# Kernel optimization log

Hardware: AMD Instinct MI355X
Metric: run time of the kernel (lower is better)

The kernel has to match this reference:

```python
import jax, jax.numpy as jnp
import numpy as np

EMBED_DIM = 1024
NUM_HEADS = 16
HEAD_DIM = EMBED_DIM // NUM_HEADS
NUM_GLOBAL = 2
NUM_RANDOM = 3
WINDOW_SIZE = 3
B, S = 2, 2048


def setup_inputs() -> dict:
    key = jax.random.key(0)
    ks = jax.random.split(key, 10)
    scale = 0.02
    inp = {
        "x": jax.random.normal(ks[0], (B, S, EMBED_DIM), dtype=jnp.float32),
        "random_indices": jax.random.randint(ks[1], (S, NUM_RANDOM), 0, S, dtype=jnp.int32),
        "q_w": jax.random.normal(ks[2], (EMBED_DIM, EMBED_DIM), dtype=jnp.float32) * scale,
        "q_b": jnp.zeros((EMBED_DIM,), dtype=jnp.float32),
        "k_w": jax.random.normal(ks[3], (EMBED_DIM, EMBED_DIM), dtype=jnp.float32) * scale,
        "k_b": jnp.zeros((EMBED_DIM,), dtype=jnp.float32),
        "v_w": jax.random.normal(ks[4], (EMBED_DIM, EMBED_DIM), dtype=jnp.float32) * scale,
        "v_b": jnp.zeros((EMBED_DIM,), dtype=jnp.float32),
        "o_w": jax.random.normal(ks[5], (EMBED_DIM, EMBED_DIM), dtype=jnp.float32) * scale,
        "o_b": jnp.zeros((EMBED_DIM,), dtype=jnp.float32),
    }
    return inp


def _build_mask(random_indices, seq_len):
    # [S, S] boolean BigBird mask: global rows/cols + sliding window + random.
    i = jnp.arange(seq_len)[:, None]
    j = jnp.arange(seq_len)[None, :]
    glob = (i < NUM_GLOBAL) | (j < NUM_GLOBAL)
    win = jnp.abs(i - j) <= WINDOW_SIZE
    rand = jnp.zeros((seq_len, seq_len), dtype=bool)
    rows = jnp.repeat(jnp.arange(seq_len), NUM_RANDOM)
    rand = rand.at[rows, random_indices.reshape(-1)].set(True)
    return glob | win | rand


def reference(x, random_indices, q_w, q_b, k_w, k_b, v_w, v_b, o_w, o_b):
    b, s, _ = x.shape
    # torch nn.Linear: y = x @ W.T + b
    q = (x @ q_w.T + q_b).reshape(b, s, NUM_HEADS, HEAD_DIM).transpose(0, 2, 1, 3)
    k = (x @ k_w.T + k_b).reshape(b, s, NUM_HEADS, HEAD_DIM).transpose(0, 2, 1, 3)
    v = (x @ v_w.T + v_b).reshape(b, s, NUM_HEADS, HEAD_DIM).transpose(0, 2, 1, 3)
    scores = jnp.einsum("bhqd,bhkd->bhqk", q, k) / jnp.sqrt(jnp.float32(HEAD_DIM))
    mask = _build_mask(random_indices, s)  # [S, S]
    scores = jnp.where(mask[None, None, :, :], scores, -jnp.inf)
    probs = jax.nn.softmax(scores, axis=-1)
    out = jnp.einsum("bhqk,bhkd->bhqd", probs, v)
    out = out.transpose(0, 2, 1, 3).reshape(b, s, EMBED_DIM)
    return out @ o_w.T + o_b
```

## Files before the change

kernel.cpp:

```cpp
#include <hip/hip_runtime.h>

#define B_  2
#define S_  2048
#define E_  1024
#define H_  16
#define D_  64
#define NGLOB 2
#define NRAND 3
#define WIN 3

typedef __bf16 bf16x8 __attribute__((ext_vector_type(8)));
typedef float  f32x4  __attribute__((ext_vector_type(4)));

__device__ __forceinline__ unsigned short f2bf(float f) {
    unsigned u = __builtin_bit_cast(unsigned, f);
    unsigned r = u + 0x7FFFu + ((u >> 16) & 1u);
    return (unsigned short)(r >> 16);
}
__device__ __forceinline__ float bf2f(unsigned short u) {
    return __builtin_bit_cast(float, (unsigned)u << 16);
}

__device__ __forceinline__ void g2l16(const unsigned short* g, unsigned short* l) {
    __builtin_amdgcn_global_load_lds(
        (const __attribute__((address_space(1))) unsigned*)g,
        (__attribute__((address_space(3))) unsigned*)l, 16, 0, 0);
}

__global__ __launch_bounds__(256)
void convert_all(const float* __restrict__ x,  const float* __restrict__ qw,
                 const float* __restrict__ kw, const float* __restrict__ vw,
                 const float* __restrict__ ow,
                 unsigned short* __restrict__ xb, unsigned short* __restrict__ wqkv,
                 unsigned short* __restrict__ wo) {
    const int XN = (B_ * S_ * E_) / 4;
    const int WN = (E_ * E_) / 4;
    int i = blockIdx.x * blockDim.x + threadIdx.x;
    int r, loc;
    if (i < XN) { r = 0; loc = i; }
    else        { int j = i - XN; r = 1 + (j >> 18); loc = j & (WN - 1); }
    const float* src = r == 0 ? x : r == 1 ? qw : r == 2 ? kw : r == 3 ? vw : ow;
    float4 f = ((const float4*)src)[loc];
    ushort4 u;
    u.x = f2bf(f.x); u.y = f2bf(f.y); u.z = f2bf(f.z); u.w = f2bf(f.w);
    ushort4* dst = r == 0 ? (ushort4*)xb : r == 4 ? (ushort4*)wo
                 : (ushort4*)wqkv + (size_t)(r - 1) * WN;
    dst[loc] = u;
}

__global__ __launch_bounds__(256, 3)
void gemm_qkv(const unsigned short* __restrict__ A,
              const unsigned short* __restrict__ W,
              const float* __restrict__ b0, const float* __restrict__ b1,
              const float* __restrict__ b2,
              unsigned short* __restrict__ Cb, int M, int N, int K) {
    __shared__ unsigned short sA[128 * 64];
    __shared__ unsigned short sB[128 * 64];
    const int t = threadIdx.x;
    const int lane = t & 63;
    const int wave = t >> 6;
    const int wm = wave >> 1, wn = wave & 1;
    const int lq = lane >> 4;
    const int lr = lane & 15;
    const int bm = blockIdx.x * 128;
    const int bn = blockIdx.y * 128;

    f32x4 acc[4][4] = {};

    for (int k0 = 0; k0 < K; k0 += 64) {
        const unsigned short* Abase = A + (size_t)bm * K + k0;
        const unsigned short* Wbase = W + (size_t)bn * K + k0;
        #pragma unroll
        for (int j = 0; j < 4; ++j) {
            int c = j * 256 + t;
            int row = c >> 3, cc = c & 7;
            int gcol = ((cc ^ (row & 7)) << 3);
            int dst = j * 2048 + wave * 512;
            g2l16(Abase + (size_t)row * K + gcol, sA + dst);
            g2l16(Wbase + (size_t)row * K + gcol, sB + dst);
        }
        __syncthreads();

        #pragma unroll
        for (int ks = 0; ks < 2; ++ks) {
            const int sw = (((ks << 2) + lq) ^ (lr & 7)) << 3;
            bf16x8 af[4], bfr[4];
            #pragma unroll
            for (int i = 0; i < 4; ++i)
                af[i] = *(const bf16x8*)&sA[(wm * 64 + i * 16 + lr) * 64 + sw];
            #pragma unroll
            for (int j = 0; j < 4; ++j)
                bfr[j] = *(const bf16x8*)&sB[(wn * 64 + j * 16 + lr) * 64 + sw];
            #pragma unroll
            for (int i = 0; i < 4; ++i)
                #pragma unroll
                for (int j = 0; j < 4; ++j)
                    acc[i][j] = __builtin_amdgcn_mfma_f32_16x16x32_bf16(af[i], bfr[j], acc[i][j], 0, 0, 0);
        }
        __syncthreads();
    }

    #pragma unroll
    for (int i = 0; i < 4; ++i) {
        int row0 = bm + wm * 64 + i * 16 + lq * 4;
        #pragma unroll
        for (int j = 0; j < 4; ++j) {
            int col = bn + wn * 64 + j * 16 + lr;
            const float* bp = col < E_ ? b0 : (col < 2 * E_ ? b1 : b2);
            float bv = bp[col & (E_ - 1)];
            #pragma unroll
            for (int r = 0; r < 4; ++r)
                Cb[(size_t)(row0 + r) * N + col] = f2bf(acc[i][j][r] + bv);
        }
    }
}

__global__ __launch_bounds__(256, 2)
void gemm_o64(const unsigned short* __restrict__ A,
              const unsigned short* __restrict__ W,
              const float* __restrict__ bias,
              float* __restrict__ Cf, int M, int N, int K) {
    __shared__ unsigned short sA[128 * 64];
    __shared__ unsigned short sB[64 * 64];
    const int t = threadIdx.x;
    const int lane = t & 63;
    const int wave = t >> 6;
    const int lq = lane >> 4;
    const int lr = lane & 15;
    const int bm = blockIdx.x * 128;
    const int bn = blockIdx.y * 64;

    f32x4 acc[2][4] = {};

    for (int k0 = 0; k0 < K; k0 += 64) {
        const unsigned short* Abase = A + (size_t)bm * K + k0;
        const unsigned short* Wbase = W + (size_t)bn * K + k0;
        #pragma unroll
        for (int j = 0; j < 4; ++j) {
            int c = j * 256 + t;
            int row = c >> 3, cc = c & 7;
            int gcol = ((cc ^ (row & 7)) << 3);
            int dst = j * 2048 + wave * 512;
            g2l16(Abase + (size_t)row * K + gcol, sA + dst);
        }
        #pragma unroll
        for (int j = 0; j < 2; ++j) {
            int c = j * 256 + t;
            int row = c >> 3, cc = c & 7;
            int gcol = ((cc ^ (row & 7)) << 3);
            int dst = j * 2048 + wave * 512;
            g2l16(Wbase + (size_t)row * K + gcol, sB + dst);
        }
        __syncthreads();

        #pragma unroll
        for (int ks = 0; ks < 2; ++ks) {
            const int sw = (((ks << 2) + lq) ^ (lr & 7)) << 3;
            bf16x8 af[2], bfr[4];
            #pragma unroll
            for (int i = 0; i < 2; ++i)
                af[i] = *(const bf16x8*)&sA[(wave * 32 + i * 16 + lr) * 64 + sw];
            #pragma unroll
            for (int j = 0; j < 4; ++j)
                bfr[j] = *(const bf16x8*)&sB[(j * 16 + lr) * 64 + sw];
            #pragma unroll
            for (int i = 0; i < 2; ++i)
                #pragma unroll
                for (int j = 0; j < 4; ++j)
                    acc[i][j] = __builtin_amdgcn_mfma_f32_16x16x32_bf16(af[i], bfr[j], acc[i][j], 0, 0, 0);
        }
        __syncthreads();
    }

    #pragma unroll
    for (int i = 0; i < 2; ++i) {
        int row0 = bm + wave * 32 + i * 16 + lq * 4;
        #pragma unroll
        for (int j = 0; j < 4; ++j) {
            int col = bn + j * 16 + lr;
            float bv = bias[col];
            #pragma unroll
            for (int r = 0; r < 4; ++r)
                Cf[(size_t)(row0 + r) * N + col] = acc[i][j][r] + bv;
        }
    }
}

__global__ __launch_bounds__(256)
void attn_fused(const unsigned short* __restrict__ qkv,
                const int* __restrict__ rnd,
                float* __restrict__ gsc, float* __restrict__ gacc,
                unsigned short* __restrict__ attn) {
    const int NB = B_ * (S_ - 2);
    int t = threadIdx.x;

    if (blockIdx.x >= 1024) {
        int bid2 = blockIdx.x - 1024;
        int tup = bid2 >> 3, seg = bid2 & 7;
        int b = tup >> 5, i = (tup >> 4) & 1, h = tup & 15;
        __shared__ float qs[D_];
        if (t < D_) qs[t] = bf2f(qkv[(size_t)(b * S_ + i) * 3072 + h * D_ + t]);
        if (seg == 0 && t < D_) gacc[tup * D_ + t] = 0.f;
        __syncthreads();
        int c = seg * 256 + t;
        const bf16x8* kp = (const bf16x8*)(qkv + (size_t)(b * S_ + c) * 3072 + E_ + h * D_);
        float s = 0.f;
        #pragma unroll
        for (int w = 0; w < 8; ++w) {
            bf16x8 kv = kp[w];
            #pragma unroll
            for (int j = 0; j < 8; ++j) s += qs[w * 8 + j] * (float)kv[j];
        }
        gsc[(size_t)tup * S_ + c] = s * 0.125f;
        return;
    }

    int bidx = (blockIdx.x & 7) * 128 + (blockIdx.x >> 3);
    int w = t >> 6, l = t & 63;
    int row = bidx * 4 + w;
    bool valid = row < NB;
    int b = row / (S_ - 2);
    int i = row % (S_ - 2) + 2;
    if (!valid) { b = 0; i = 2; }

    __shared__ int   cols_s[4][12];
    __shared__ int   ncol_sh[4];
    __shared__ float pr_s[4][16 * 13 + 3];

    const bf16x8* qp = (const bf16x8*)(qkv + (size_t)(b * S_ + i) * 3072);
    bf16x8 q0 = qp[l * 2], q1 = qp[l * 2 + 1];
    float qreg[16];
    #pragma unroll
    for (int j = 0; j < 8; ++j) { qreg[j] = (float)q0[j]; qreg[8 + j] = (float)q1[j]; }

    if (l == 0) {
        int* cols = cols_s[w];
        int n = 0;
        cols[n++] = 0; cols[n++] = 1;
        int lo = i - WIN; if (lo < NGLOB) lo = NGLOB;
        int hi = i + WIN; if (hi > S_ - 1) hi = S_ - 1;
        for (int j = lo; j <= hi; ++j) cols[n++] = j;
        for (int r = 0; r < NRAND; ++r) {
            int c = rnd[i * NRAND + r];
            bool dup = false;
            for (int q = 0; q < n; ++q) dup = dup || (cols[q] == c);
            if (!dup) cols[n++] = c;
        }
        ncol_sh[w] = n;
        for (int q = n; q < 12; ++q) cols[q] = 0;
    }
    __syncthreads();
    const int n = ncol_sh[w];
    const int h4 = l >> 2;

    float sco[12];
    #pragma unroll
    for (int c = 0; c < 12; ++c) {
        const bf16x8* kp = (const bf16x8*)(qkv + (size_t)(b * S_ + cols_s[w][c]) * 3072 + E_);
        bf16x8 k0 = kp[l * 2], k1 = kp[l * 2 + 1];
        float s = 0.f;
        #pragma unroll
        for (int j = 0; j < 8; ++j) s += qreg[j] * (float)k0[j] + qreg[8 + j] * (float)k1[j];
        s += __shfl_xor(s, 1);
        s += __shfl_xor(s, 2);
        sco[c] = (c < n) ? s * 0.125f : -1e30f;
    }

    if ((l & 3) == 0) {
        float m = -1e30f;
        #pragma unroll
        for (int c = 0; c < 12; ++c) m = fmaxf(m, sco[c]);
        float sum = 0.f;
        #pragma unroll
        for (int c = 0; c < 12; ++c) { float e = __expf(sco[c] - m); sco[c] = e; sum += e; }
        float inv = 1.f / sum;
        #pragma unroll
        for (int c = 0; c < 12; ++c) pr_s[w][h4 * 13 + c] = sco[c] * inv;
    }
    __syncthreads();

    float o[16] = {};
    #pragma unroll
    for (int c = 0; c < 12; ++c) {
        float p = pr_s[w][h4 * 13 + c];
        const bf16x8* vp = (const bf16x8*)(qkv + (size_t)(b * S_ + cols_s[w][c]) * 3072 + 2 * E_);
        bf16x8 v0 = vp[l * 2], v1 = vp[l * 2 + 1];
        #pragma unroll
        for (int j = 0; j < 8; ++j) { o[j] += p * (float)v0[j]; o[8 + j] += p * (float)v1[j]; }
    }

    if (valid) {
        ushort4 u0, u1, u2, u3;
        u0.x = f2bf(o[0]);  u0.y = f2bf(o[1]);  u0.z = f2bf(o[2]);  u0.w = f2bf(o[3]);
        u1.x = f2bf(o[4]);  u1.y = f2bf(o[5]);  u1.z = f2bf(o[6]);  u1.w = f2bf(o[7]);
        u2.x = f2bf(o[8]);  u2.y = f2bf(o[9]);  u2.z = f2bf(o[10]); u2.w = f2bf(o[11]);
        u3.x = f2bf(o[12]); u3.y = f2bf(o[13]); u3.z = f2bf(o[14]); u3.w = f2bf(o[15]);
        ushort4* op = (ushort4*)(attn + (size_t)(b * S_ + i) * E_ + l * 16);
        op[0] = u0; op[1] = u1; op[2] = u2; op[3] = u3;
    }
}

__global__ __launch_bounds__(256)
void gattn_pv(const unsigned short* __restrict__ qkv, const float* __restrict__ gsc,
              float* __restrict__ gacc) {
    int tup = blockIdx.x, chunk = blockIdx.y;
    int b = tup >> 5, h = tup & 15;
    int t = threadIdx.x, w = t >> 6, d = t & 63;
    __shared__ float ps[S_];
    __shared__ float red[4];
    __shared__ float redv[4][D_];
    const float* sc = gsc + (size_t)tup * S_;

    float vals[8];
    float m = -1e30f;
    #pragma unroll
    for (int k = 0; k < 8; ++k) { vals[k] = sc[t + 256 * k]; m = fmaxf(m, vals[k]); }
    #pragma unroll
    for (int o = 32; o; o >>= 1) m = fmaxf(m, __shfl_down(m, o));
    if ((t & 63) == 0) red[t >> 6] = m;
    __syncthreads();
    m = fmaxf(fmaxf(red[0], red[1]), fmaxf(red[2], red[3]));
    __syncthreads();
    float sum = 0.f;
    #pragma unroll
    for (int k = 0; k < 8; ++k) { float e = __expf(vals[k] - m); vals[k] = e; sum += e; }
    #pragma unroll
    for (int o = 32; o; o >>= 1) sum += __shfl_down(sum, o);
    if ((t & 63) == 0) red[t >> 6] = sum;
    __syncthreads();
    float inv = 1.f / (red[0] + red[1] + red[2] + red[3]);
    #pragma unroll
    for (int k = 0; k < 8; ++k) ps[t + 256 * k] = vals[k] * inv;
    __syncthreads();

    const float* P = ps + chunk * 256 + w * 64;
    float acc = 0.f;
    #pragma unroll 4
    for (int k = 0; k < 64; ++k) {
        int c = chunk * 256 + w * 64 + k;
        acc += P[k] * bf2f(qkv[(size_t)(b * S_ + c) * 3072 + 2 * E_ + h * D_ + d]);
    }
    redv[w][d] = acc;
    __syncthreads();
    if (w == 0)
        atomicAdd(&gacc[tup * D_ + d], redv[0][d] + redv[1][d] + redv[2][d] + redv[3][d]);
}

__global__ __launch_bounds__(256)
void gattn_fin(const float* __restrict__ gacc, unsigned short* __restrict__ attn) {
    int gid = blockIdx.x * 256 + threadIdx.x;
    int tup = gid >> 6, d = gid & 63;
    int b = tup >> 5, i = (tup >> 4) & 1, h = tup & 15;
    attn[(size_t)(b * S_ + i) * E_ + h * D_ + d] = f2bf(gacc[gid]);
}

extern "C" void kernel_launch(void* const* d_in, const int* in_sizes, int n_in,
                              void* d_out, int out_size, void* d_ws, size_t ws_size,
                              hipStream_t stream) {
    const float* x   = (const float*)d_in[0];
    const int*   rnd = (const int*)d_in[1];
    const float* qw  = (const float*)d_in[2];
    const float* qb  = (const float*)d_in[3];
    const float* kw  = (const float*)d_in[4];
    const float* kb  = (const float*)d_in[5];
    const float* vw  = (const float*)d_in[6];
    const float* vb  = (const float*)d_in[7];
    const float* ow  = (const float*)d_in[8];
    const float* ob  = (const float*)d_in[9];
    float* out = (float*)d_out;

    char* ws = (char*)d_ws;
    unsigned short* xb    = (unsigned short*)(ws);
    unsigned short* wqkv  = (unsigned short*)(ws + 8388608);
    unsigned short* wo    = (unsigned short*)(ws + 14680064);
    unsigned short* qkv   = (unsigned short*)(ws + 16777216);
    unsigned short* attn  = (unsigned short*)(ws + 41943040);
    float*          gsc   = (float*)(ws);
    float*          gacc  = (float*)(ws + 524288);

    const int M = B_ * S_;

    {
        int total4 = (M * E_ + 4 * E_ * E_) / 4;
        convert_all<<<total4 / 256, 256, 0, stream>>>(x, qw, kw, vw, ow, xb, wqkv, wo);
    }

    {
        dim3 grid(M / 128, 3 * E_ / 128);
        gemm_qkv<<<grid, 256, 0, stream>>>(xb, wqkv, qb, kb, vb, qkv, M, 3 * E_, E_);
    }

    attn_fused<<<1024 + 512, 256, 0, stream>>>(qkv, rnd, gsc, gacc, attn);

    gattn_pv<<<dim3(B_ * NGLOB * H_, S_ / 256), 256, 0, stream>>>(qkv, gsc, gacc);
    gattn_fin<<<(B_ * NGLOB * H_ * D_) / 256, 256, 0, stream>>>(gacc, attn);

    {
        dim3 grid(M / 128, E_ / 64);
        gemm_o64<<<grid, 256, 0, stream>>>(attn, wo, ob, out, M, E_, E_);
    }
}
```

Measured before the change: 173.1 us.

## Restructure QKV GEMM into 256x256 tile double-buffered pipelined kernel

```diff
diff --git a/kernel.cpp b/kernel.cpp
--- a/kernel.cpp
+++ b/kernel.cpp
@@ -48,69 +48,158 @@
     dst[loc] = u;
 }
 
-__global__ __launch_bounds__(256, 3)
+__device__ __forceinline__ void stage_half(const unsigned short* g, unsigned short* l,
+                                           int t, int wave, int K) {
+    #pragma unroll
+    for (int j = 0; j < 2; ++j) {
+        int c = j * 512 + t;
+        int row = c >> 3, cc = c & 7;
+        g2l16(g + (size_t)row * K + ((cc ^ (row & 7)) << 3), l + j * 4096 + wave * 512);
+    }
+}
+__device__ __forceinline__ bf16x8 ldfrag(const unsigned short* r, int row, int kc) {
+    return *(const bf16x8*)&r[row * 64 + ((kc ^ (row & 7)) << 3)];
+}
+
+__global__ __launch_bounds__(512, 2)
 void gemm_qkv(const unsigned short* __restrict__ A,
               const unsigned short* __restrict__ W,
-              const float* __restrict__ b0, const float* __restrict__ b1,
-              const float* __restrict__ b2,
+              const float* __restrict__ bi0, const float* __restrict__ bi1,
+              const float* __restrict__ bi2,
               unsigned short* __restrict__ Cb, int M, int N, int K) {
-    __shared__ unsigned short sA[128 * 64];
-    __shared__ unsigned short sB[128 * 64];
+    __shared__ unsigned short lds[2][4][128 * 64];
     const int t = threadIdx.x;
     const int lane = t & 63;
     const int wave = t >> 6;
-    const int wm = wave >> 1, wn = wave & 1;
+    const int wr = wave >> 2;
+    const int wc = wave & 3;
     const int lq = lane >> 4;
     const int lr = lane & 15;
-    const int bm = blockIdx.x * 128;
-    const int bn = blockIdx.y * 128;
-
-    f32x4 acc[4][4] = {};
-
-    for (int k0 = 0; k0 < K; k0 += 64) {
-        const unsigned short* Abase = A + (size_t)bm * K + k0;
-        const unsigned short* Wbase = W + (size_t)bn * K + k0;
-        #pragma unroll
-        for (int j = 0; j < 4; ++j) {
-            int c = j * 256 + t;
-            int row = c >> 3, cc = c & 7;
-            int gcol = ((cc ^ (row & 7)) << 3);
-            int dst = j * 2048 + wave * 512;
-            g2l16(Abase + (size_t)row * K + gcol, sA + dst);
-            g2l16(Wbase + (size_t)row * K + gcol, sB + dst);
-        }
-        __syncthreads();
-
-        #pragma unroll
-        for (int ks = 0; ks < 2; ++ks) {
-            const int sw = (((ks << 2) + lq) ^ (lr & 7)) << 3;
-            bf16x8 af[4], bfr[4];
-            #pragma unroll
-            for (int i = 0; i < 4; ++i)
-                af[i] = *(const bf16x8*)&sA[(wm * 64 + i * 16 + lr) * 64 + sw];
-            #pragma unroll
-            for (int j = 0; j < 4; ++j)
-                bfr[j] = *(const bf16x8*)&sB[(wn * 64 + j * 16 + lr) * 64 + sw];
-            #pragma unroll
-            for (int i = 0; i < 4; ++i)
+    const int bm = blockIdx.x * 256;
+    const int bn = blockIdx.y * 256;
+    const int nt = K >> 6;
+
+    const unsigned short* Ab = A + (size_t)bm * K;
+    const unsigned short* Wb = W + (size_t)bn * K;
+
+    f32x4 acc[8][4] = {};
+
+    stage_half(Ab,                         &lds[0][0][0], t, wave, K);
+    stage_half(Ab + (size_t)128 * K,       &lds[0][1][0], t, wave, K);
+    stage_half(Wb,                         &lds[0][2][0], t, wave, K);
+    stage_half(Wb + (size_t)128 * K,       &lds[0][3][0], t, wave, K);
+    stage_half(Wb + 64,                    &lds[1][2][0], t, wave, K);
+    stage_half(Wb + (size_t)128 * K + 64,  &lds[1][3][0], t, wave, K);
+    asm volatile("s_waitcnt vmcnt(4)" ::: "memory");
+    __builtin_amdgcn_s_barrier();
+
+    #pragma unroll 2
+    for (int kt = 0; kt < nt; ++kt) {
+        const int cur = kt & 1;
+        const unsigned short* rA = &lds[cur][wr][0];
+        const unsigned short* rB = &lds[cur][2 + (wc >> 1)][0];
+        const int brow = (wc & 1) * 64;
+        bf16x8 af[2][2], bfr[4][2];
+
+        #pragma unroll
+        for (int m = 0; m < 2; ++m)
+            #pragma unroll
+            for (int ks = 0; ks < 2; ++ks)
+                af[m][ks] = ldfrag(rA, m * 16 + lr, ks * 4 + lq);
+        #pragma unroll
+        for (int n = 0; n < 4; ++n)
+            #pragma unroll
+            for (int ks = 0; ks < 2; ++ks)
+                bfr[n][ks] = ldfrag(rB, brow + n * 16 + lr, ks * 4 + lq);
+        if (kt + 1 < nt)
+            stage_half(Ab + (size_t)(kt + 1) * 64, &lds[cur ^ 1][0][0], t, wave, K);
+        __builtin_amdgcn_s_barrier();
+        asm volatile("s_waitcnt lgkmcnt(0)" ::: "memory");
+        __builtin_amdgcn_s_setprio(1);
+        #pragma unroll
+        for (int m = 0; m < 2; ++m)
+            #pragma unroll
+            for (int n = 0; n < 4; ++n)
                 #pragma unroll
-                for (int j = 0; j < 4; ++j)
-                    acc[i][j] = __builtin_amdgcn_mfma_f32_16x16x32_bf16(af[i], bfr[j], acc[i][j], 0, 0, 0);
-        }
-        __syncthreads();
-    }
-
-    #pragma unroll
-    for (int i = 0; i < 4; ++i) {
-        int row0 = bm + wm * 64 + i * 16 + lq * 4;
-        #pragma unroll
-        for (int j = 0; j < 4; ++j) {
-            int col = bn + wn * 64 + j * 16 + lr;
-            const float* bp = col < E_ ? b0 : (col < 2 * E_ ? b1 : b2);
+                for (int ks = 0; ks < 2; ++ks)
+                    acc[m][n] = __builtin_amdgcn_mfma_f32_16x16x32_bf16(af[m][ks], bfr[n][ks], acc[m][n], 0, 0, 0);
+        __builtin_amdgcn_s_setprio(0);
+        __builtin_amdgcn_s_barrier();
+
+        #pragma unroll
+        for (int m = 0; m < 2; ++m)
+            #pragma unroll
+            for (int ks = 0; ks < 2; ++ks)
+                af[m][ks] = ldfrag(rA, (2 + m) * 16 + lr, ks * 4 + lq);
+        if (kt + 1 < nt)
+            stage_half(Ab + (size_t)128 * K + (size_t)(kt + 1) * 64, &lds[cur ^ 1][1][0], t, wave, K);
+        if (kt + 2 < nt)
+            stage_half(Wb + (size_t)(kt + 2) * 64, &lds[cur][2][0], t, wave, K);
+        __builtin_amdgcn_s_barrier();
+        asm volatile("s_waitcnt lgkmcnt(0)" ::: "memory");
+        __builtin_amdgcn_s_setprio(1);
+        #pragma unroll
+        for (int m = 0; m < 2; ++m)
+            #pragma unroll
+            for (int n = 0; n < 4; ++n)
+                #pragma unroll
+                for (int ks = 0; ks < 2; ++ks)
+                    acc[2 + m][n] = __builtin_amdgcn_mfma_f32_16x16x32_bf16(af[m][ks], bfr[n][ks], acc[2 + m][n], 0, 0, 0);
+        __builtin_amdgcn_s_setprio(0);
+        __builtin_amdgcn_s_barrier();
+
+        #pragma unroll
+        for (int m = 0; m < 2; ++m)
+            #pragma unroll
+            for (int ks = 0; ks < 2; ++ks)
+                af[m][ks] = ldfrag(rA, (4 + m) * 16 + lr, ks * 4 + lq);
+        if (kt + 2 < nt)
+            stage_half(Wb + (size_t)128 * K + (size_t)(kt + 2) * 64, &lds[cur][3][0], t, wave, K);
+        __builtin_amdgcn_s_barrier();
+        asm volatile("s_waitcnt lgkmcnt(0)" ::: "memory");
+        __builtin_amdgcn_s_setprio(1);
+        #pragma unroll
+        for (int m = 0; m < 2; ++m)
+            #pragma unroll
+            for (int n = 0; n < 4; ++n)
+                #pragma unroll
+                for (int ks = 0; ks < 2; ++ks)
+                    acc[4 + m][n] = __builtin_amdgcn_mfma_f32_16x16x32_bf16(af[m][ks], bfr[n][ks], acc[4 + m][n], 0, 0, 0);
+        __builtin_amdgcn_s_setprio(0);
+        __builtin_amdgcn_s_barrier();
+
+        #pragma unroll
+        for (int m = 0; m < 2; ++m)
+            #pragma unroll
+            for (int ks = 0; ks < 2; ++ks)
+                af[m][ks] = ldfrag(rA, (6 + m) * 16 + lr, ks * 4 + lq);
+        __builtin_amdgcn_s_barrier();
+        asm volatile("s_waitcnt lgkmcnt(0)" ::: "memory");
+        __builtin_amdgcn_s_setprio(1);
+        #pragma unroll
+        for (int m = 0; m < 2; ++m)
+            #pragma unroll
+            for (int n = 0; n < 4; ++n)
+                #pragma unroll
+                for (int ks = 0; ks < 2; ++ks)
+                    acc[6 + m][n] = __builtin_amdgcn_mfma_f32_16x16x32_bf16(af[m][ks], bfr[n][ks], acc[6 + m][n], 0, 0, 0);
+        __builtin_amdgcn_s_setprio(0);
+        if (kt + 2 < nt) asm volatile("s_waitcnt vmcnt(4)" ::: "memory");
+        else             asm volatile("s_waitcnt vmcnt(0)" ::: "memory");
+        __builtin_amdgcn_s_barrier();
+    }
+
+    #pragma unroll
+    for (int m = 0; m < 8; ++m) {
+        int row0 = bm + wr * 128 + m * 16 + lq * 4;
+        #pragma unroll
+        for (int n = 0; n < 4; ++n) {
+            int col = bn + wc * 64 + n * 16 + lr;
+            const float* bp = col < E_ ? bi0 : (col < 2 * E_ ? bi1 : bi2);
             float bv = bp[col & (E_ - 1)];
             #pragma unroll
             for (int r = 0; r < 4; ++r)
-                Cb[(size_t)(row0 + r) * N + col] = f2bf(acc[i][j][r] + bv);
+                Cb[(size_t)(row0 + r) * N + col] = f2bf(acc[m][n][r] + bv);
         }
     }
 }
@@ -386,8 +475,8 @@
     }
 
     {
-        dim3 grid(M / 128, 3 * E_ / 128);
-        gemm_qkv<<<grid, 256, 0, stream>>>(xb, wqkv, qb, kb, vb, qkv, M, 3 * E_, E_);
+        dim3 grid(M / 256, 3 * E_ / 256);
+        gemm_qkv<<<grid, 512, 0, stream>>>(xb, wqkv, qb, kb, vb, qkv, M, 3 * E_, E_);
     }
 
     attn_fused<<<1024 + 512, 256, 0, stream>>>(qkv, rnd, gsc, gacc, attn);
```

Result: slower. 176.7 us (+2.1%).

## Fuse global-row attention into attn_fused, removing separate PV and finalize kernels

Applied to the files above, without the earlier changes.

```diff
diff --git a/kernel.cpp b/kernel.cpp
--- a/kernel.cpp
+++ b/kernel.cpp
@@ -189,33 +189,71 @@
 __global__ __launch_bounds__(256)
 void attn_fused(const unsigned short* __restrict__ qkv,
                 const int* __restrict__ rnd,
-                float* __restrict__ gsc, float* __restrict__ gacc,
                 unsigned short* __restrict__ attn) {
     const int NB = B_ * (S_ - 2);
     int t = threadIdx.x;
 
-    if (blockIdx.x >= 1024) {
-        int bid2 = blockIdx.x - 1024;
-        int tup = bid2 >> 3, seg = bid2 & 7;
+    if (blockIdx.x < 64) {
+        int tup = blockIdx.x;
         int b = tup >> 5, i = (tup >> 4) & 1, h = tup & 15;
+        int w = t >> 6, l = t & 63;
         __shared__ float qs[D_];
+        __shared__ float ps[S_];
+        __shared__ float red[4];
+        __shared__ float ov[4][D_];
         if (t < D_) qs[t] = bf2f(qkv[(size_t)(b * S_ + i) * 3072 + h * D_ + t]);
-        if (seg == 0 && t < D_) gacc[tup * D_ + t] = 0.f;
-        __syncthreads();
-        int c = seg * 256 + t;
-        const bf16x8* kp = (const bf16x8*)(qkv + (size_t)(b * S_ + c) * 3072 + E_ + h * D_);
-        float s = 0.f;
-        #pragma unroll
-        for (int w = 0; w < 8; ++w) {
-            bf16x8 kv = kp[w];
-            #pragma unroll
-            for (int j = 0; j < 8; ++j) s += qs[w * 8 + j] * (float)kv[j];
-        }
-        gsc[(size_t)tup * S_ + c] = s * 0.125f;
+        __syncthreads();
+
+        float vals[8];
+        float m = -1e30f;
+        #pragma unroll
+        for (int kk = 0; kk < 8; ++kk) {
+            int c = kk * 256 + t;
+            const bf16x8* kp = (const bf16x8*)(qkv + (size_t)(b * S_ + c) * 3072 + E_ + h * D_);
+            float s = 0.f;
+            #pragma unroll
+            for (int u = 0; u < 8; ++u) {
+                bf16x8 kv = kp[u];
+                #pragma unroll
+                for (int j = 0; j < 8; ++j) s += qs[u * 8 + j] * (float)kv[j];
+            }
+            vals[kk] = s * 0.125f;
+            m = fmaxf(m, vals[kk]);
+        }
+        #pragma unroll
+        for (int o = 32; o; o >>= 1) m = fmaxf(m, __shfl_down(m, o));
+        if (l == 0) red[w] = m;
+        __syncthreads();
+        m = fmaxf(fmaxf(red[0], red[1]), fmaxf(red[2], red[3]));
+        __syncthreads();
+        float sum = 0.f;
+        #pragma unroll
+        for (int kk = 0; kk < 8; ++kk) { float e = __expf(vals[kk] - m); vals[kk] = e; sum += e; }
+        #pragma unroll
+        for (int o = 32; o; o >>= 1) sum += __shfl_down(sum, o);
+        if (l == 0) red[w] = sum;
+        __syncthreads();
+        float inv = 1.f / (red[0] + red[1] + red[2] + red[3]);
+        #pragma unroll
+        for (int kk = 0; kk < 8; ++kk) ps[kk * 256 + t] = vals[kk] * inv;
+        __syncthreads();
+
+        const unsigned short* vbase = qkv + (size_t)(b * S_ + w * 512) * 3072 + 2 * E_ + h * D_ + l;
+        const float* pw = ps + w * 512;
+        float acc = 0.f;
+        #pragma unroll 8
+        for (int k = 0; k < 512; ++k)
+            acc += pw[k] * bf2f(vbase[(size_t)k * 3072]);
+        ov[w][l] = acc;
+        __syncthreads();
+        if (w == 0)
+            attn[(size_t)(b * S_ + i) * E_ + h * D_ + l] =
+                f2bf(ov[0][l] + ov[1][l] + ov[2][l] + ov[3][l]);
         return;
     }
 
-    int bidx = (blockIdx.x & 7) * 128 + (blockIdx.x >> 3);
+    int bb = blockIdx.x - 64;
+    int bidx = (bb & 7) * 128 + (bb >> 3);
     int w = t >> 6, l = t & 63;
     int row = bidx * 4 + w;
     bool valid = row < NB;
@@ -298,60 +336,6 @@
         ushort4* op = (ushort4*)(attn + (size_t)(b * S_ + i) * E_ + l * 16);
         op[0] = u0; op[1] = u1; op[2] = u2; op[3] = u3;
     }
-}
-
-__global__ __launch_bounds__(256)
-void gattn_pv(const unsigned short* __restrict__ qkv, const float* __restrict__ gsc,
-              float* __restrict__ gacc) {
-    int tup = blockIdx.x, chunk = blockIdx.y;
-    int b = tup >> 5, h = tup & 15;
-    int t = threadIdx.x, w = t >> 6, d = t & 63;
-    __shared__ float ps[S_];
-    __shared__ float red[4];
-    __shared__ float redv[4][D_];
-    const float* sc = gsc + (size_t)tup * S_;
-
-    float vals[8];
-    float m = -1e30f;
-    #pragma unroll
-    for (int k = 0; k < 8; ++k) { vals[k] = sc[t + 256 * k]; m = fmaxf(m, vals[k]); }
-    #pragma unroll
-    for (int o = 32; o; o >>= 1) m = fmaxf(m, __shfl_down(m, o));
-    if ((t & 63) == 0) red[t >> 6] = m;
-    __syncthreads();
-    m = fmaxf(fmaxf(red[0], red[1]), fmaxf(red[2], red[3]));
-    __syncthreads();
-    float sum = 0.f;
-    #pragma unroll
-    for (int k = 0; k < 8; ++k) { float e = __expf(vals[k] - m); vals[k] = e; sum += e; }
-    #pragma unroll
-    for (int o = 32; o; o >>= 1) sum += __shfl_down(sum, o);
-    if ((t & 63) == 0) red[t >> 6] = sum;
-    __syncthreads();
-    float inv = 1.f / (red[0] + red[1] + red[2] + red[3]);
-    #pragma unroll
-    for (int k = 0; k < 8; ++k) ps[t + 256 * k] = vals[k] * inv;
-    __syncthreads();
-
-    const float* P = ps + chunk * 256 + w * 64;
-    float acc = 0.f;
-    #pragma unroll 4
-    for (int k = 0; k < 64; ++k) {
-        int c = chunk * 256 + w * 64 + k;
-        acc += P[k] * bf2f(qkv[(size_t)(b * S_ + c) * 3072 + 2 * E_ + h * D_ + d]);
-    }
-    redv[w][d] = acc;
-    __syncthreads();
-    if (w == 0)
-        atomicAdd(&gacc[tup * D_ + d], redv[0][d] + redv[1][d] + redv[2][d] + redv[3][d]);
-}
-
-__global__ __launch_bounds__(256)
-void gattn_fin(const float* __restrict__ gacc, unsigned short* __restrict__ attn) {
-    int gid = blockIdx.x * 256 + threadIdx.x;
-    int tup = gid >> 6, d = gid & 63;
-    int b = tup >> 5, i = (tup >> 4) & 1, h = tup & 15;
-    attn[(size_t)(b * S_ + i) * E_ + h * D_ + d] = f2bf(gacc[gid]);
 }
 
 extern "C" void kernel_launch(void* const* d_in, const int* in_sizes, int n_in,
@@ -375,8 +359,6 @@
     unsigned short* wo    = (unsigned short*)(ws + 14680064);
     unsigned short* qkv   = (unsigned short*)(ws + 16777216);
     unsigned short* attn  = (unsigned short*)(ws + 41943040);
-    float*          gsc   = (float*)(ws);
-    float*          gacc  = (float*)(ws + 524288);
 
     const int M = B_ * S_;
 
@@ -390,10 +372,7 @@
         gemm_qkv<<<grid, 256, 0, stream>>>(xb, wqkv, qb, kb, vb, qkv, M, 3 * E_, E_);
     }
 
-    attn_fused<<<1024 + 512, 256, 0, stream>>>(qkv, rnd, gsc, gacc, attn);
-
-    gattn_pv<<<dim3(B_ * NGLOB * H_, S_ / 256), 256, 0, stream>>>(qkv, gsc, gacc);
-    gattn_fin<<<(B_ * NGLOB * H_ * D_) / 256, 256, 0, stream>>>(gacc, attn);
+    attn_fused<<<64 + 1024, 256, 0, stream>>>(qkv, rnd, attn);
 
     {
         dim3 grid(M / 128, E_ / 64);
```

Result: slower. 186.4 us (+7.7%).
